# Performance work log

Measured on AMD Instinct MI355X. Metric: run time of the kernel, lower is better.

Reference implementation:

```python
import jax, jax.numpy as jnp
import numpy as np

N_EMBD = 1024
N_HEAD = 16

def setup_inputs() -> dict:
    key = jax.random.key(0)
    ks = jax.random.split(key, 5)
    B, T, C = 4, 2048, N_EMBD
    s = 0.02
    return {
        'x': jax.random.normal(ks[0], (B, T, C), jnp.float32),
        'w_attn': jax.random.normal(ks[1], (C, 3 * C), jnp.float32) * s,
        'b_attn': jax.random.normal(ks[2], (3 * C,), jnp.float32) * s,
        'w_proj': jax.random.normal(ks[3], (C, C), jnp.float32) * s,
        'b_proj': jax.random.normal(ks[4], (C,), jnp.float32) * s,
    }

def reference(x, w_attn, b_attn, w_proj, b_proj):
    B, T, C = x.shape
    H = N_HEAD
    D = C // H  # head dim
    qkv = x @ w_attn + b_attn                      # [B,T,3C]
    q, k, v = jnp.split(qkv, 3, axis=-1)
    q = q.reshape(B, T, H, D).transpose(0, 2, 1, 3)  # [B,H,T,D]
    k = k.reshape(B, T, H, D).transpose(0, 2, 1, 3)
    v = v.reshape(B, T, H, D).transpose(0, 2, 1, 3)
    att = jnp.einsum('bhqd,bhkd->bhqk', q, k) * (1.0 / jnp.sqrt(jnp.float32(D)))
    causal = jnp.tril(jnp.ones((T, T), bool))
    att = jnp.where(causal[None, None], att, jnp.float32(-jnp.inf))
    att = jax.nn.softmax(att, axis=-1)
    y = jnp.einsum('bhqk,bhkd->bhqd', att, v)      # [B,H,T,D]
    y = y.transpose(0, 2, 1, 3).reshape(B, T, C)
    return y @ w_proj + b_proj
```

## Files before the change

### kernel.cpp

```cpp
#include <hip/hip_runtime.h>
#include <math.h>

typedef short s16x8 __attribute__((ext_vector_type(8)));
typedef unsigned short u16;
typedef unsigned short u16x4 __attribute__((ext_vector_type(4)));
typedef float f32x4 __attribute__((ext_vector_type(4)));

__device__ __forceinline__ f32x4 mfma16(s16x8 a, s16x8 b, f32x4 c) {
  return __builtin_amdgcn_mfma_f32_16x16x32_bf16(a, b, c, 0, 0, 0);
}

__device__ __forceinline__ u16 f2bf(float f) {
  unsigned u = __builtin_bit_cast(unsigned, f);
  u = (u + 0x7fffu + ((u >> 16) & 1u)) >> 16;
  return (u16)u;
}

__device__ __forceinline__ unsigned pk_trunc(float hi, float lo) {
  return __builtin_amdgcn_perm(__builtin_bit_cast(unsigned, hi),
                               __builtin_bit_cast(unsigned, lo), 0x07060302u);
}

__device__ __forceinline__ s16x8 mk_pa(unsigned a, unsigned b, unsigned c, unsigned d) {
  union { unsigned u[4]; s16x8 h; } t;
  t.u[0] = a; t.u[1] = b; t.u[2] = c; t.u[3] = d;
  return t.h;
}

__device__ __forceinline__ void gll16(const void* g, void* l) {
  __builtin_amdgcn_global_load_lds((__attribute__((address_space(1))) void*)(void*)g,
                                   (__attribute__((address_space(3))) void*)l,
                                   16, 0, 0);
}

__device__ __forceinline__ void transpose_body(const float* __restrict__ in,
                                               u16* __restrict__ out, int R, int C,
                                               int bx, int by, float (*tile)[33]) {
  int c0 = bx * 32, r0 = by * 32;
  int tx = threadIdx.x & 31, ty = threadIdx.x >> 5;
#pragma unroll
  for (int s = 0; s < 4; ++s)
    tile[ty + 8 * s][tx] = in[(size_t)(r0 + ty + 8 * s) * C + c0 + tx];
  __syncthreads();
#pragma unroll
  for (int s = 0; s < 4; ++s)
    out[(size_t)(c0 + ty + 8 * s) * R + r0 + tx] = f2bf(tile[tx][ty + 8 * s]);
}

__global__ __launch_bounds__(256) void k_prep(const float* __restrict__ x,
                                              u16* __restrict__ xb,
                                              const float* __restrict__ w_attn,
                                              u16* __restrict__ waT,
                                              const float* __restrict__ w_proj,
                                              u16* __restrict__ wpT) {
  __shared__ float tile[32][33];
  int id = blockIdx.x;
  if (id < 4096) {
    int i = (id * 256 + threadIdx.x) * 8;
    const float4* xv = (const float4*)(x + i);
    float4 a = xv[0], b = xv[1];
    union { s16x8 v; u16 s[8]; } r;
    r.s[0] = f2bf(a.x); r.s[1] = f2bf(a.y); r.s[2] = f2bf(a.z); r.s[3] = f2bf(a.w);
    r.s[4] = f2bf(b.x); r.s[5] = f2bf(b.y); r.s[6] = f2bf(b.z); r.s[7] = f2bf(b.w);
    *(s16x8*)(xb + i) = r.v;
  } else if (id < 4096 + 3072) {
    int t = id - 4096;
    transpose_body(w_attn, waT, 1024, 3072, t % 96, t / 96, tile);
  } else {
    int t = id - (4096 + 3072);
    transpose_body(w_proj, wpT, 1024, 1024, t % 32, t / 32, tile);
  }
}

template <int EPI>
__global__ __launch_bounds__(256) void k_gemm(const u16* __restrict__ A,
                                              const u16* __restrict__ Bt,
                                              const float* __restrict__ bias,
                                              float* __restrict__ outp,
                                              u16* __restrict__ q_out,
                                              u16* __restrict__ k_out,
                                              u16* __restrict__ vt_out,
                                              int K, int nIter) {
  __shared__ u16 As[2][4096];
  __shared__ u16 Bs[2][4096];
  int tid = threadIdx.x, w = tid >> 6, l = tid & 63;
  int r = l & 15, qd = l >> 4;
  int id = blockIdx.x;
  int xcd = id & 7, s0 = id >> 3;
  int mBlk = xcd * 8 + (s0 & 7);
  int nBlk = s0 >> 3;
  f32x4 acc[4][4] = {};

  const u16* ga[2]; const u16* gb[2]; int lgrp[2];
#pragma unroll
  for (int qq = 0; qq < 2; ++qq) {
    int grp = 2 * w + qq;
    int rowA = mBlk * 128 + grp * 16 + (l >> 2);
    int rowB = nBlk * 128 + grp * 16 + (l >> 2);
    int kcol = (l & 3) * 8;
    ga[qq] = A + (size_t)rowA * K + kcol;
    gb[qq] = Bt + (size_t)rowB * K + kcol;
    lgrp[qq] = grp * 512;
  }
  int aoff = ((w & 1) * 4) * 512 + r * 32 + qd * 8;
  int boff = ((w >> 1) * 4) * 512 + r * 32 + qd * 8;

  auto stageg = [&](int kt, int buf) {
#pragma unroll
    for (int qq = 0; qq < 2; ++qq) {
      gll16(ga[qq] + kt * 32, As[buf] + lgrp[qq]);
      gll16(gb[qq] + kt * 32, Bs[buf] + lgrp[qq]);
    }
  };

  stageg(0, 0);
  __syncthreads();

  for (int kt = 0; kt < nIter; ++kt) {
    int cur = kt & 1;
    if (kt + 1 < nIter) stageg(kt + 1, cur ^ 1);
    s16x8 af[4], bf[4];
#pragma unroll
    for (int i = 0; i < 4; ++i) af[i] = *(const s16x8*)(As[cur] + aoff + i * 512);
#pragma unroll
    for (int j = 0; j < 4; ++j) bf[j] = *(const s16x8*)(Bs[cur] + boff + j * 512);
#pragma unroll
    for (int i = 0; i < 4; ++i)
#pragma unroll
      for (int j = 0; j < 4; ++j) acc[i][j] = mfma16(af[i], bf[j], acc[i][j]);
    __syncthreads();
  }

  const float QSCALE = 0.125f * 1.44269504088896f;
  int rowBase = mBlk * 128 + (w & 1) * 64;
  int colBase = nBlk * 128 + (w >> 1) * 64;
#pragma unroll
  for (int i = 0; i < 4; ++i) {
#pragma unroll
    for (int j = 0; j < 4; ++j) {
      int col = colBase + j * 16 + r;
      float bv = bias[col];
      float vv[4];
#pragma unroll
      for (int g = 0; g < 4; ++g) vv[g] = acc[i][j][g] + bv;
      int row0 = rowBase + i * 16 + qd * 4;
      if (EPI == 0) {
        int which = col >> 10;
        int rem = col & 1023;
        int hh = rem >> 6, dd = rem & 63;
        int bb = row0 >> 11, tt0 = row0 & 2047;
        if (which == 2) {
          u16x4 pk;
#pragma unroll
          for (int g = 0; g < 4; ++g) pk[g] = f2bf(vv[g]);
          *(u16x4*)(vt_out + (((size_t)(bb * 16 + hh)) * 64 + dd) * 2048 + tt0) = pk;
        } else {
          u16* base = (which == 0) ? q_out : k_out;
#pragma unroll
          for (int g = 0; g < 4; ++g) {
            float v = vv[g];
            if (which == 0) v *= QSCALE;
            base[(((size_t)(bb * 16 + hh)) * 2048 + tt0 + g) * 64 + dd] = f2bf(v);
          }
        }
      } else {
#pragma unroll
        for (int g = 0; g < 4; ++g)
          outp[(size_t)(row0 + g) * 1024 + col] = vv[g];
      }
    }
  }
}

__global__ __launch_bounds__(256, 4) void k_attn(const u16* __restrict__ qg,
                                                 const u16* __restrict__ kg,
                                                 const u16* __restrict__ vtg,
                                                 u16* __restrict__ yg) {
  __shared__ u16 Ks[2][64 * 64];
  __shared__ u16 Vs[2][64 * 64];

  int id = blockIdx.x;
  int xcd = id & 7;
  int slot = id >> 3;
  int bx = slot & 15;
  int bh = ((slot >> 4) << 3) | xcd;
  int bb = bh >> 4, hh = bh & 15;
  int tid = threadIdx.x, w = tid >> 6, l = tid & 63;
  int r = l & 15, qd = l >> 4;

  const int chunk0 = bx, chunk1 = 31 - bx;
  int nmax = 32 - bx;
  int qloc = w * 16 + r;

  s16x8 qf[2][2];
#pragma unroll
  for (int c = 0; c < 2; ++c) {
    int qbase = (c ? chunk1 : chunk0) * 64 + w * 16;
#pragma unroll
    for (int s = 0; s < 2; ++s)
      qf[c][s] = *(const s16x8*)(qg + ((size_t)bh * 2048 + qbase + r) * 64 + s * 32 + qd * 8);
  }

  s16x8 onesf;
#pragma unroll
  for (int e = 0; e < 8; ++e) onesf[e] = (short)0x3F80;

  f32x4 o[2][4] = {};
  f32x4 lacc[2] = {};

  int rl = l >> 3;
  int cg = (l & 7) ^ rl;
  const u16* kbase = kg + (size_t)bh * 2048 * 64;
  const u16* vbase = vtg + (size_t)bh * 64 * 2048;

  auto stage = [&](int kt, int buf) {
    int kk0 = kt * 64;
#pragma unroll
    for (int p = 0; p < 2; ++p) {
      int row = p * 32 + w * 8 + rl;
      gll16(kbase + ((size_t)(kk0 + row)) * 64 + cg * 8, Ks[buf] + p * 2048 + w * 512);
      gll16(vbase + (size_t)row * 2048 + kk0 + cg * 8, Vs[buf] + p * 2048 + w * 512);
    }
  };

  auto smax = [&](f32x4 (&sc)[4], s16x8 (&pac)[2], bool mask) {
    unsigned pk[4][2];
#pragma unroll
    for (int j = 0; j < 4; ++j) {
      float p0, p1, p2, p3;
      if (mask) {
        int kb0 = 16 * j + 4 * qd;
        p0 = (kb0 + 0 > qloc) ? 0.f : __builtin_amdgcn_exp2f(sc[j][0]);
        p1 = (kb0 + 1 > qloc) ? 0.f : __builtin_amdgcn_exp2f(sc[j][1]);
        p2 = (kb0 + 2 > qloc) ? 0.f : __builtin_amdgcn_exp2f(sc[j][2]);
        p3 = (kb0 + 3 > qloc) ? 0.f : __builtin_amdgcn_exp2f(sc[j][3]);
      } else {
        p0 = __builtin_amdgcn_exp2f(sc[j][0]);
        p1 = __builtin_amdgcn_exp2f(sc[j][1]);
        p2 = __builtin_amdgcn_exp2f(sc[j][2]);
        p3 = __builtin_amdgcn_exp2f(sc[j][3]);
      }
      pk[j][0] = pk_trunc(p1, p0);
      pk[j][1] = pk_trunc(p3, p2);
    }
#pragma unroll
    for (int s = 0; s < 2; ++s) {
      unsigned a0 = pk[2 * s][0], b0 = pk[2 * s + 1][0];
      asm("v_permlane32_swap_b32 %0, %1" : "+v"(a0), "+v"(b0));
      asm("v_permlane16_swap_b32 %0, %1" : "+v"(a0), "+v"(b0));
      unsigned a1 = pk[2 * s][1], b1 = pk[2 * s + 1][1];
      asm("v_permlane32_swap_b32 %0, %1" : "+v"(a1), "+v"(b1));
      asm("v_permlane16_swap_b32 %0, %1" : "+v"(a1), "+v"(b1));
      pac[s] = mk_pa(a0, a1, b0, b1);
    }
  };

  stage(0, 0);
  __syncthreads();

  for (int kt = 0; kt < nmax; ++kt) {
    int cur = kt & 1;
    if (kt + 1 < nmax) stage(kt + 1, cur ^ 1);
    bool act0 = (kt <= bx);

    f32x4 s0[4], s1[4];
#pragma unroll
    for (int j = 0; j < 4; ++j) {
      s1[j] = f32x4{0.f, 0.f, 0.f, 0.f};
      if (act0) s0[j] = f32x4{0.f, 0.f, 0.f, 0.f};
    }
    __builtin_amdgcn_s_setprio(1);
#pragma unroll
    for (int s = 0; s < 2; ++s) {
#pragma unroll
      for (int j = 0; j < 4; ++j) {
        s16x8 kf = *(const s16x8*)(Ks[cur] + (16 * j + r) * 64 + ((s * 4 + qd) ^ (r & 7)) * 8);
        s1[j] = mfma16(kf, qf[1][s], s1[j]);
        if (act0) s0[j] = mfma16(kf, qf[0][s], s0[j]);
      }
    }
    __builtin_amdgcn_s_setprio(0);

    s16x8 pa0[2], pa1[2];
    smax(s1, pa1, kt == chunk1);
    lacc[1] = mfma16(onesf, pa1[0], lacc[1]);
    lacc[1] = mfma16(onesf, pa1[1], lacc[1]);
    if (act0) {
      smax(s0, pa0, kt == chunk0);
      lacc[0] = mfma16(onesf, pa0[0], lacc[0]);
      lacc[0] = mfma16(onesf, pa0[1], lacc[0]);
    }

    __builtin_amdgcn_s_setprio(1);
#pragma unroll
    for (int s = 0; s < 2; ++s) {
#pragma unroll
      for (int j = 0; j < 4; ++j) {
        s16x8 vf = *(const s16x8*)(Vs[cur] + (16 * j + r) * 64 + ((s * 4 + qd) ^ (r & 7)) * 8);
        o[1][j] = mfma16(vf, pa1[s], o[1][j]);
        if (act0) o[0][j] = mfma16(vf, pa0[s], o[0][j]);
      }
    }
    __builtin_amdgcn_s_setprio(0);

    __syncthreads();
  }

#pragma unroll
  for (int c = 0; c < 2; ++c) {
    int qbase = (c ? chunk1 : chunk0) * 64 + w * 16;
    float inv = 1.0f / lacc[c][0];
    size_t rowoff = ((size_t)bb * 2048 + qbase + r) * 1024 + hh * 64;
#pragma unroll
    for (int j = 0; j < 4; ++j) {
      u16x4 yv;
      yv[0] = f2bf(o[c][j][0] * inv);
      yv[1] = f2bf(o[c][j][1] * inv);
      yv[2] = f2bf(o[c][j][2] * inv);
      yv[3] = f2bf(o[c][j][3] * inv);
      *(u16x4*)(yg + rowoff + 16 * j + 4 * qd) = yv;
    }
  }
}

extern "C" void kernel_launch(void* const* d_in, const int* in_sizes, int n_in,
                              void* d_out, int out_size, void* d_ws, size_t ws_size,
                              hipStream_t stream) {
  const float* x      = (const float*)d_in[0];
  const float* w_attn = (const float*)d_in[1];
  const float* b_attn = (const float*)d_in[2];
  const float* w_proj = (const float*)d_in[3];
  const float* b_proj = (const float*)d_in[4];
  float* out = (float*)d_out;

  char* ws = (char*)d_ws;
  size_t off = 0;
  auto alloc = [&](size_t bytes) -> void* {
    void* p = ws + off;
    off += (bytes + 255) & ~(size_t)255;
    return p;
  };
  const size_t BT = 8192, C = 1024;
  u16* xb  = (u16*)alloc(BT * C * 2);
  u16* waT = (u16*)alloc(3072 * 1024 * 2);
  u16* wpT = (u16*)alloc(1024 * 1024 * 2);
  u16* qb  = (u16*)alloc(BT * C * 2);
  u16* kb  = (u16*)alloc(BT * C * 2);
  u16* vtb = (u16*)alloc(BT * C * 2);
  (void)ws_size; (void)in_sizes; (void)n_in; (void)out_size;

  k_prep<<<4096 + 3072 + 1024, 256, 0, stream>>>(x, xb, w_attn, waT, w_proj, wpT);
  k_gemm<0><<<1536, 256, 0, stream>>>(xb, waT, b_attn, nullptr, qb, kb, vtb, 1024, 32);
  k_attn<<<1024, 256, 0, stream>>>(qb, kb, vtb, xb );
  k_gemm<1><<<512, 256, 0, stream>>>(xb, wpT, b_proj, out, nullptr, nullptr, nullptr, 1024, 32);
}
```

Measured before the change: 243.7 us.

## Use smaller-tile projection GEMM and compute softmax row sums with VALU adds

Adds a dedicated output-projection GEMM with 128x64 tiles launched on 1024 blocks, replacing the generic 512-block GEMM. The goal is better CU occupancy and load balance on the final projection. In attention, the per-row denominator is now accumulated with scalar adds and cross-lane shuffles instead of extra MFMA ops against a ones matrix. This frees matrix-core issue slots, at the cost of some VALU work and a different summation precision (fp32 before bf16 truncation).

```diff
diff --git a/kernel.cpp b/kernel.cpp
--- a/kernel.cpp
+++ b/kernel.cpp
@@ -172,6 +172,68 @@
   }
 }
 
+__global__ __launch_bounds__(256) void k_gemmP(const u16* __restrict__ A,
+                                               const u16* __restrict__ Bt,
+                                               const float* __restrict__ bias,
+                                               float* __restrict__ outp) {
+  __shared__ u16 As[2][128 * 32];
+  __shared__ u16 Bs[2][64 * 32];
+  const int K = 1024;
+  int tid = threadIdx.x, w = tid >> 6, l = tid & 63;
+  int r = l & 15, qd = l >> 4;
+  int wm = w >> 1, wn = w & 1;
+  int id = blockIdx.x;
+  int xcd = id & 7, s0 = id >> 3;
+  int mBlk = xcd * 8 + (s0 & 7);
+  int nBlk = s0 >> 3;
+  f32x4 acc[4][2] = {};
+
+  int kcol = (tid & 3) * 8;
+  const u16* ga = A + (size_t)(mBlk * 128 + (tid >> 2)) * K + kcol;
+  const u16* gb = Bt + (size_t)(nBlk * 64 + (tid >> 2)) * K + kcol;
+  int aoff = (wm * 64 + r) * 32 + qd * 8;
+  int boff = (wn * 32 + r) * 32 + qd * 8;
+
+  auto stageg = [&](int kt, int buf) {
+    gll16(ga + kt * 32, (char*)As[buf] + w * 1024);
+    gll16(ga + (size_t)64 * K + kt * 32, (char*)As[buf] + 4096 + w * 1024);
+    gll16(gb + kt * 32, (char*)Bs[buf] + w * 1024);
+  };
+
+  stageg(0, 0);
+  __syncthreads();
+
+  for (int kt = 0; kt < 32; ++kt) {
+    int cur = kt & 1;
+    if (kt + 1 < 32) stageg(kt + 1, cur ^ 1);
+    s16x8 af[4], bf[2];
+#pragma unroll
+    for (int i = 0; i < 4; ++i) af[i] = *(const s16x8*)(As[cur] + aoff + i * 512);
+#pragma unroll
+    for (int j = 0; j < 2; ++j) bf[j] = *(const s16x8*)(Bs[cur] + boff + j * 512);
+#pragma unroll
+    for (int i = 0; i < 4; ++i)
+#pragma unroll
+      for (int j = 0; j < 2; ++j) acc[i][j] = mfma16(af[i], bf[j], acc[i][j]);
+    __syncthreads();
+  }
+
+  int rowBase = mBlk * 128 + wm * 64;
+  int colBase = nBlk * 64 + wn * 32;
+#pragma unroll
+  for (int i = 0; i < 4; ++i) {
+#pragma unroll
+    for (int j = 0; j < 2; ++j) {
+      int col = colBase + j * 16 + r;
+      float bv = bias[col];
+      int row0 = rowBase + i * 16 + qd * 4;
+#pragma unroll
+      for (int g = 0; g < 4; ++g)
+        outp[(size_t)(row0 + g) * 1024 + col] = acc[i][j][g] + bv;
+    }
+  }
+}
+
 __global__ __launch_bounds__(256, 4) void k_attn(const u16* __restrict__ qg,
                                                  const u16* __restrict__ kg,
                                                  const u16* __restrict__ vtg,
@@ -201,12 +263,8 @@
       qf[c][s] = *(const s16x8*)(qg + ((size_t)bh * 2048 + qbase + r) * 64 + s * 32 + qd * 8);
   }
 
-  s16x8 onesf;
-#pragma unroll
-  for (int e = 0; e < 8; ++e) onesf[e] = (short)0x3F80;
-
   f32x4 o[2][4] = {};
-  f32x4 lacc[2] = {};
+  float lsum[2] = {0.f, 0.f};
 
   int rl = l >> 3;
   int cg = (l & 7) ^ rl;
@@ -223,7 +281,7 @@
     }
   };
 
-  auto smax = [&](f32x4 (&sc)[4], s16x8 (&pac)[2], bool mask) {
+  auto smax = [&](f32x4 (&sc)[4], s16x8 (&pac)[2], bool mask, float& sum) {
     unsigned pk[4][2];
 #pragma unroll
     for (int j = 0; j < 4; ++j) {
@@ -240,6 +298,7 @@
         p2 = __builtin_amdgcn_exp2f(sc[j][2]);
         p3 = __builtin_amdgcn_exp2f(sc[j][3]);
       }
+      sum += (p0 + p1) + (p2 + p3);
       pk[j][0] = pk_trunc(p1, p0);
       pk[j][1] = pk_trunc(p3, p2);
     }
@@ -282,14 +341,8 @@
     __builtin_amdgcn_s_setprio(0);
 
     s16x8 pa0[2], pa1[2];
-    smax(s1, pa1, kt == chunk1);
-    lacc[1] = mfma16(onesf, pa1[0], lacc[1]);
-    lacc[1] = mfma16(onesf, pa1[1], lacc[1]);
-    if (act0) {
-      smax(s0, pa0, kt == chunk0);
-      lacc[0] = mfma16(onesf, pa0[0], lacc[0]);
-      lacc[0] = mfma16(onesf, pa0[1], lacc[0]);
-    }
+    smax(s1, pa1, kt == chunk1, lsum[1]);
+    if (act0) smax(s0, pa0, kt == chunk0, lsum[0]);
 
     __builtin_amdgcn_s_setprio(1);
 #pragma unroll
@@ -309,7 +362,10 @@
 #pragma unroll
   for (int c = 0; c < 2; ++c) {
     int qbase = (c ? chunk1 : chunk0) * 64 + w * 16;
-    float inv = 1.0f / lacc[c][0];
+    float tot = lsum[c];
+    tot += __shfl_xor(tot, 16);
+    tot += __shfl_xor(tot, 32);
+    float inv = 1.0f / tot;
     size_t rowoff = ((size_t)bb * 2048 + qbase + r) * 1024 + hh * 64;
 #pragma unroll
     for (int j = 0; j < 4; ++j) {
@@ -352,5 +408,5 @@
   k_prep<<<4096 + 3072 + 1024, 256, 0, stream>>>(x, xb, w_attn, waT, w_proj, wpT);
   k_gemm<0><<<1536, 256, 0, stream>>>(xb, waT, b_attn, nullptr, qb, kb, vtb, 1024, 32);
   k_attn<<<1024, 256, 0, stream>>>(qb, kb, vtb, xb );
-  k_gemm<1><<<512, 256, 0, stream>>>(xb, wpT, b_proj, out, nullptr, nullptr, nullptr, 1024, 32);
-}
+  k_gemmP<<<1024, 256, 0, stream>>>(xb, wpT, b_proj, out);
+}
```

After: 244.8 us (median of 2 runs). Within noise of the previous version (+0.5%).
